# Performance work log

Measured on AMD Instinct MI355X. Metric: run time of the kernel, lower is better.

## Reference

```python
import jax, jax.numpy as jnp
import numpy as np
import math

B, C, MX, MY, MZ = 4, 64, 32, 32, 32
N_ATOM, EMB, N_HEAD = 64, 128, 8
HEAD = C // N_HEAD


def setup_inputs() -> dict:
    key = jax.random.key(0)
    ks = jax.random.split(key, 12)
    s = 0.05
    return {
        "x": jax.random.normal(ks[0], (B, C, MX, MY, MZ), jnp.float32),
        "mol_embed": jax.random.normal(ks[1], (B, N_ATOM, EMB), jnp.float32),
        "batch_nodes": jax.random.randint(ks[2], (B,), 1, N_ATOM + 1),  # >=1 valid atom
        "Wq": jax.random.normal(ks[3], (C, C), jnp.float32) * s,
        "bq": jnp.zeros((C,), jnp.float32),
        "Wk": jax.random.normal(ks[4], (C, EMB), jnp.float32) * s,
        "bk": jnp.zeros((C,), jnp.float32),
        "Wv": jax.random.normal(ks[5], (C, EMB), jnp.float32) * s,
        "bv": jnp.zeros((C,), jnp.float32),
        "Wo": jax.random.normal(ks[6], (C, C), jnp.float32) * s,
        "bo": jnp.zeros((C,), jnp.float32),
        "Wc": jax.random.normal(ks[7], (C, C, 3, 3, 3), jnp.float32) * s,
        "bc": jnp.zeros((C,), jnp.float32),
    }


def reference(x, mol_embed, batch_nodes, Wq, bq, Wk, bk, Wv, bv, Wo, bo, Wc, bc):
    b, c, mx, my, mz = x.shape
    m_voxel = mx * my * mz
    n_atom = mol_embed.shape[1]
    x_in = x

    # [b, m_voxel, c] voxel tokens
    xt = x.reshape(b, c, m_voxel).transpose(0, 2, 1)
    q = (xt @ Wq.T + bq).reshape(b, m_voxel, N_HEAD, HEAD)
    k = (mol_embed @ Wk.T + bk).reshape(b, n_atom, N_HEAD, HEAD)
    v = (mol_embed @ Wv.T + bv).reshape(b, n_atom, N_HEAD, HEAD)

    att = jnp.einsum('bqhd,bkhd->bhqk', q, k) / math.sqrt(HEAD)
    # ragged per-batch masking: atoms >= batch_nodes[i] are invalid
    valid = jnp.arange(n_atom)[None, :] < batch_nodes[:, None]  # [b, n_atom]
    att = jnp.where(valid[:, None, None, :], att, -jnp.inf)
    att = jax.nn.softmax(att, axis=-1)

    o = jnp.einsum('bhqk,bkhd->bqhd', att, v).reshape(b, m_voxel, c)
    o = jax.nn.relu(o @ Wo.T + bo)
    o = o.transpose(0, 2, 1).reshape(b, c, mx, my, mz)

    # conv3d k=3 with circular padding
    op = jnp.pad(o, ((0, 0), (0, 0), (1, 1), (1, 1), (1, 1)), mode='wrap')
    conv = jax.lax.conv_general_dilated(
        op, Wc, window_strides=(1, 1, 1), padding='VALID',
        dimension_numbers=('NCDHW', 'OIDHW', 'NCDHW'))
    conv = conv + bc[None, :, None, None, None]
    return jax.nn.relu(conv) + x_in
```

## Files before the change

### kernel.cpp

```cpp
#include <hip/hip_runtime.h>
#include <hip/hip_bf16.h>

#define B_    4
#define C_    64
#define MVOX  32768
#define NATOM 64
#define EMB_  128

typedef __attribute__((ext_vector_type(8)))  __bf16 bf16x8;
typedef __attribute__((ext_vector_type(4)))  float  f32x4;
typedef __attribute__((ext_vector_type(16))) float  f32x16;
typedef __attribute__((ext_vector_type(8)))  unsigned short ushort8;

typedef __attribute__((address_space(1))) const unsigned int gas_u32;
typedef __attribute__((address_space(3))) unsigned int las_u32;

static __device__ __forceinline__ unsigned short bf16u(float f) {
  __hip_bfloat16 h = __float2bfloat16(f);
  return *(unsigned short*)&h;
}

__global__ __launch_bounds__(256) void wprep_kernel(
    const float* __restrict__ Wc, const float* __restrict__ Wq,
    const float* __restrict__ Wo, const float* __restrict__ Wk,
    const float* __restrict__ Wv,
    __hip_bfloat16* __restrict__ Wt4, __hip_bfloat16* __restrict__ Wqb,
    __hip_bfloat16* __restrict__ Wob, __hip_bfloat16* __restrict__ Wkb,
    __hip_bfloat16* __restrict__ Wvb) {
  const int i = blockIdx.x * 256 + threadIdx.x;
  if (i < 110592) {
    const int tap = i >> 12;
    const int coh = (i >> 11) & 1;
    const int ks  = (i >> 9) & 3;
    const int l   = (i >> 3) & 63;
    const int j   = i & 7;
    const int co  = coh * 32 + (l & 31);
    const int ci  = ks * 16 + ((l >> 5) << 3) + j;
    Wt4[i] = __float2bfloat16(Wc[(co * C_ + ci) * 27 + tap]);
  } else if (i < 114688) {
    const int i2 = i - 110592;
    const int nf = (i2 >> 10) & 3;
    const int kk = (i2 >> 9) & 1;
    const int l  = (i2 >> 3) & 63;
    const int j  = i2 & 7;
    const int co = nf * 16 + (l & 15);
    const int ci = kk * 32 + ((l >> 4) << 3) + j;
    Wqb[i2] = __float2bfloat16(Wq[co * C_ + ci] * 0.3535533905932738f);
  } else if (i < 118784) {
    const int i3 = i - 114688;
    const int nf = (i3 >> 10) & 3;
    const int kk = (i3 >> 9) & 1;
    const int l  = (i3 >> 3) & 63;
    const int j  = i3 & 7;
    const int co = nf * 16 + (l & 15);
    const int ci = kk * 32 + ((l >> 4) << 3) + j;
    Wob[i3] = __float2bfloat16(Wo[co * C_ + ci]);
  } else if (i < 135168) {
    const int i4 = (i - 118784) & 8191;
    const bool is_v = (i - 118784) >= 8192;
    const int ch = i4 >> 12;
    const int kk = (i4 >> 9) & 7;
    const int l  = (i4 >> 3) & 63;
    const int j  = i4 & 7;
    const int c  = ch * 32 + (l & 31);
    const int e  = kk * 16 + ((l >> 5) << 3) + j;
    const float v = (is_v ? Wv : Wk)[c * EMB_ + e];
    (is_v ? Wvb : Wkb)[i4] = __float2bfloat16(v);
  }
}

__global__ __launch_bounds__(256) void kv_kernel(
    const float* __restrict__ mol,
    const __hip_bfloat16* __restrict__ Wkb, const float* __restrict__ bk,
    const __hip_bfloat16* __restrict__ Wvb, const float* __restrict__ bv,
    float* __restrict__ kout, float* __restrict__ vout) {
  __shared__ float smol[NATOM][132];

  const int b    = blockIdx.x;
  const int tid  = threadIdx.x;
  const int lane = tid & 63;
  const int w    = tid >> 6;
  const int kv   = w >> 1;
  const int ah   = w & 1;

  for (int i = tid; i < 2048; i += 256) {
    const int a = i >> 4, cb = (i & 15) * 8;
    const f32x4 v0 = *(const f32x4*)&mol[(size_t)(b * NATOM + a) * EMB_ + cb];
    const f32x4 v1 = *(const f32x4*)&mol[(size_t)(b * NATOM + a) * EMB_ + cb + 4];
    *(f32x4*)&smol[a][cb]     = v0;
    *(f32x4*)&smol[a][cb + 4] = v1;
  }
  __syncthreads();

  const __hip_bfloat16* Wb   = kv ? Wvb : Wkb;
  const float*          bias = kv ? bv : bk;
  float*                out  = kv ? vout : kout;

  f32x16 acc[2];
  #pragma unroll
  for (int ch = 0; ch < 2; ++ch)
    #pragma unroll
    for (int r = 0; r < 16; ++r) acc[ch][r] = 0.f;

  const int a  = ah * 32 + (lane & 31);
  #pragma unroll
  for (int kk = 0; kk < 8; ++kk) {
    const int e0 = kk * 16 + ((lane >> 5) << 3);
    ushort8 au;
    #pragma unroll
    for (int j = 0; j < 8; ++j) au[j] = bf16u(smol[a][e0 + j]);
    const bf16x8 af = __builtin_bit_cast(bf16x8, au);
    #pragma unroll
    for (int ch = 0; ch < 2; ++ch) {
      const bf16x8 bf = *(const bf16x8*)(Wb + (((ch * 8 + kk) << 6) + lane) * 8);
      acc[ch] = __builtin_amdgcn_mfma_f32_32x32x16_bf16(af, bf, acc[ch], 0, 0, 0);
    }
  }

  #pragma unroll
  for (int ch = 0; ch < 2; ++ch) {
    const int c = ch * 32 + (lane & 31);
    const float bb = bias[c];
    #pragma unroll
    for (int r = 0; r < 16; ++r) {
      const int ar = ah * 32 + (r & 3) + 8 * (r >> 2) + 4 * (lane >> 5);
      out[(size_t)(b * NATOM + ar) * C_ + c] = acc[ch][r] + bb;
    }
  }
}

__global__ __launch_bounds__(512, 4) void attn_kernel(
    const float* __restrict__ x,
    const float* __restrict__ kbuf, const float* __restrict__ vbuf,
    const int* __restrict__ batch_nodes,
    const __hip_bfloat16* __restrict__ Wqb, const float* __restrict__ bq,
    const __hip_bfloat16* __restrict__ Wob, const float* __restrict__ bo,
    __hip_bfloat16* __restrict__ omid) {
  __shared__ float sk[NATOM * C_];
  __shared__ float sv[NATOM * C_];
  __shared__ float xq[64 * C_];

  const int b    = blockIdx.y;
  const int m0   = blockIdx.x * 64;
  const int tid  = threadIdx.x;
  const int lane = tid & 63;
  const int w    = __builtin_amdgcn_readfirstlane(tid >> 6);
  const int h    = w;
  const int quad = lane >> 4;
  const int l15  = lane & 15;
  const int vq   = w & 3;
  const int cq   = w >> 2;

  #pragma unroll
  for (int j = 0; j < 2; ++j) {
    const int cidx = w * 2 + j;
    const int c  = cidx * 4 + (lane >> 4);
    const int v4 = (lane & 15) * 4;
    const float* gsrc = x + (size_t)(b * C_ + c) * MVOX + m0 + v4;
    __builtin_amdgcn_global_load_lds((gas_u32*)gsrc,
                                     (las_u32*)&xq[cidx * 256], 16, 0, 0);
  }
  for (int i = tid; i < NATOM * C_; i += 512) {
    const int at = i >> 6, c = i & 63;
    const int ad = (at << 6) + ((((c >> 2) ^ (at & 15)) << 2)) + (c & 3);
    sk[ad] = kbuf[b * NATOM * C_ + i];
    sv[ad] = vbuf[b * NATOM * C_ + i];
  }
  __syncthreads();

  f32x4 qacc[2];
  {
    bf16x8 af[2];
    #pragma unroll
    for (int kk = 0; kk < 2; ++kk) {
      ushort8 au;
      #pragma unroll
      for (int j = 0; j < 8; ++j)
        au[j] = bf16u(xq[(kk * 32 + quad * 8 + j) * 64 + vq * 16 + l15]);
      af[kk] = __builtin_bit_cast(bf16x8, au);
    }
    #pragma unroll
    for (int nf2 = 0; nf2 < 2; ++nf2) {
      const int nf = cq * 2 + nf2;
      const float bqv = bq[nf * 16 + l15] * 0.3535533905932738f;
      qacc[nf2] = {bqv, bqv, bqv, bqv};
      #pragma unroll
      for (int kk = 0; kk < 2; ++kk) {
        const bf16x8 bf = *(const bf16x8*)(Wqb + (((nf * 2 + kk) << 6) + lane) * 8);
        qacc[nf2] = __builtin_amdgcn_mfma_f32_16x16x32_bf16(af[kk], bf, qacc[nf2], 0, 0, 0);
      }
    }
  }
  __syncthreads();

  #pragma unroll
  for (int nf2 = 0; nf2 < 2; ++nf2) {
    const int co = (cq * 2 + nf2) * 16 + l15;
    const int c4 = co >> 2, ce = co & 3;
    #pragma unroll
    for (int r = 0; r < 4; ++r) {
      const int vr = vq * 16 + quad * 4 + r;
      xq[vr * 64 + ((c4 ^ (vr & 15)) << 2) + ce] = qacc[nf2][r];
    }
  }
  __syncthreads();

  const int nv = batch_nodes[b];

  bf16x8 kf[4];
  #pragma unroll
  for (int a = 0; a < 4; ++a) {
    const int arow = a * 16 + l15;
    const f32x4 k0 = *(const f32x4*)&sk[arow * 64 + (((2 * h)     ^ l15) << 2)];
    const f32x4 k1 = *(const f32x4*)&sk[arow * 64 + (((2 * h + 1) ^ l15) << 2)];
    ushort8 au;
    #pragma unroll
    for (int j = 0; j < 4; ++j) {
      au[j]     = (quad == 0) ? bf16u(k0[j]) : (unsigned short)0;
      au[4 + j] = (quad == 0) ? bf16u(k1[j]) : (unsigned short)0;
    }
    kf[a] = __builtin_bit_cast(bf16x8, au);
  }
  bf16x8 vf[2];
  {
    const int vc  = h * 8 + (l15 & 7);
    const int vc4 = vc >> 2, vce = vc & 3;
    #pragma unroll
    for (int s = 0; s < 2; ++s) {
      ushort8 au;
      #pragma unroll
      for (int j = 0; j < 8; ++j) {
        const int atom = (2 * s + (j >> 2)) * 16 + quad * 4 + (j & 3);
        au[j] = bf16u(sv[(atom << 6) + ((vc4 ^ (atom & 15)) << 2) + vce]);
      }
      vf[s] = __builtin_bit_cast(bf16x8, au);
    }
  }

  f32x4 oacc[4];
  #pragma unroll
  for (int v = 0; v < 4; ++v)
    #pragma unroll
    for (int r = 0; r < 4; ++r) oacc[v][r] = 0.f;

  const f32x4 zero4 = {0.f, 0.f, 0.f, 0.f};
  #pragma unroll
  for (int v = 0; v < 4; ++v) {
    const int qrow = v * 16 + l15;
    const f32x4 q0 = *(const f32x4*)&xq[qrow * 64 + (((2 * h)     ^ l15) << 2)];
    const f32x4 q1 = *(const f32x4*)&xq[qrow * 64 + (((2 * h + 1) ^ l15) << 2)];
    ushort8 qu;
    #pragma unroll
    for (int j = 0; j < 4; ++j) { qu[j] = bf16u(q0[j]); qu[4 + j] = bf16u(q1[j]); }
    const bf16x8 qf = __builtin_bit_cast(bf16x8, qu);

    f32x4 st[4];
    #pragma unroll
    for (int a = 0; a < 4; ++a)
      st[a] = __builtin_amdgcn_mfma_f32_16x16x32_bf16(kf[a], qf, zero4, 0, 0, 0);

    float m = -1e30f;
    #pragma unroll
    for (int a = 0; a < 4; ++a)
      #pragma unroll
      for (int r = 0; r < 4; ++r) {
        const int atom = a * 16 + quad * 4 + r;
        const float val = (atom < nv) ? st[a][r] : -1e30f;
        st[a][r] = val;
        m = fmaxf(m, val);
      }
    m = fmaxf(m, __shfl_xor(m, 16, 64));
    m = fmaxf(m, __shfl_xor(m, 32, 64));
    float ssum = 0.f;
    #pragma unroll
    for (int a = 0; a < 4; ++a)
      #pragma unroll
      for (int r = 0; r < 4; ++r) {
        const float p = __expf(st[a][r] - m);
        st[a][r] = p;
        ssum += p;
      }
    ssum += __shfl_xor(ssum, 16, 64);
    ssum += __shfl_xor(ssum, 32, 64);
    const float inv = 1.f / ssum;

    #pragma unroll
    for (int s = 0; s < 2; ++s) {
      ushort8 pu;
      #pragma unroll
      for (int j = 0; j < 8; ++j)
        pu[j] = bf16u(st[2 * s + (j >> 2)][j & 3] * inv);
      const bf16x8 pa = __builtin_bit_cast(bf16x8, pu);
      oacc[v] = __builtin_amdgcn_mfma_f32_16x16x32_bf16(pa, vf[s], oacc[v], 0, 0, 0);
    }
  }
  __syncthreads();

  float* os = sk;
  if (l15 < 8) {
    const int c = h * 8 + l15;
    const int c4 = c >> 2, ce = c & 3;
    #pragma unroll
    for (int v = 0; v < 4; ++v)
      #pragma unroll
      for (int r = 0; r < 4; ++r) {
        const int vxr = v * 16 + quad * 4 + r;
        os[vxr * 64 + ((c4 ^ (vxr & 15)) << 2) + ce] = oacc[v][r];
      }
  }
  __syncthreads();

  {
    bf16x8 af[2];
    #pragma unroll
    for (int kk = 0; kk < 2; ++kk) {
      ushort8 au;
      #pragma unroll
      for (int j = 0; j < 8; ++j) {
        const int ci = kk * 32 + quad * 8 + j;
        const int c4 = ci >> 2;
        au[j] = bf16u(os[(vq * 16 + l15) * 64 + ((c4 ^ l15) << 2) + (ci & 3)]);
      }
      af[kk] = __builtin_bit_cast(bf16x8, au);
    }
    f32x4 oac[2];
    #pragma unroll
    for (int nf2 = 0; nf2 < 2; ++nf2) {
      const int nf = cq * 2 + nf2;
      const float bov = bo[nf * 16 + l15];
      oac[nf2] = {bov, bov, bov, bov};
      #pragma unroll
      for (int kk = 0; kk < 2; ++kk) {
        const bf16x8 bf = *(const bf16x8*)(Wob + (((nf * 2 + kk) << 6) + lane) * 8);
        oac[nf2] = __builtin_amdgcn_mfma_f32_16x16x32_bf16(af[kk], bf, oac[nf2], 0, 0, 0);
      }
    }
    __syncthreads();
    unsigned short* osb = (unsigned short*)xq;
    #pragma unroll
    for (int nf2 = 0; nf2 < 2; ++nf2) {
      const int co = (cq * 2 + nf2) * 16 + l15;
      #pragma unroll
      for (int r = 0; r < 4; ++r) {
        const int vr = vq * 16 + quad * 4 + r;
        osb[vr * 64 + (((co >> 3) ^ (vr & 7)) << 3) + (co & 7)] =
            bf16u(fmaxf(oac[nf2][r], 0.f));
      }
    }
  }
  __syncthreads();

  *(ushort8*)(omid + (size_t)(b * MVOX + m0) * C_ + tid * 8) =
      *(const ushort8*)&((unsigned short*)xq)[tid * 8];
}

#define LOADB(dst, DX, DY, DZ)                                              \
  {                                                                         \
    const int zp_ = ((lane & 31) + (DZ) + 31) & 31;                         \
    const int sw_ = zp_ & 7;                                                \
    _Pragma("unroll")                                                       \
    for (int ks_ = 0; ks_ < 4; ++ks_) {                                     \
      const int phys_ = (ks_ * 2 + (lane >> 5)) ^ sw_;                      \
      _Pragma("unroll")                                                     \
      for (int i_ = 0; i_ < 2; ++i_) {                                      \
        const int hl_ = (lp + (DX)) * 4 + (i_ + (DY));                      \
        (dst)[i_ * 4 + ks_] =                                               \
            *(const bf16x8*)&halo[((hl_ * 32 + zp_) * 8 + phys_) * 8];      \
      }                                                                     \
    }                                                                       \
  }

#define LOADW(T2)                                                           \
  _Pragma("unroll")                                                         \
  for (int ks_ = 0; ks_ < 4; ++ks_)                                         \
    wf[(T2) % 3][ks_] =                                                     \
        *(const bf16x8*)(Wt4 + ((((T2) * 2 + coh) * 4 + ks_) << 9) + lane * 8);

#define DOMFMA(src, T)                                                      \
  _Pragma("unroll")                                                         \
  for (int ks_ = 0; ks_ < 4; ++ks_)                                         \
    _Pragma("unroll")                                                       \
    for (int i_ = 0; i_ < 2; ++i_)                                          \
      acc[i_] = __builtin_amdgcn_mfma_f32_32x32x16_bf16(                    \
          wf[(T) % 3][ks_], (src)[i_ * 4 + ks_], acc[i_], 0, 0, 0);

__global__ __launch_bounds__(256, 2) void conv_kernel(
    const __hip_bfloat16* __restrict__ omid,
    const __hip_bfloat16* __restrict__ Wt4,
    const float* __restrict__ bc,
    const float* __restrict__ xin,
    float* __restrict__ out) {
  __shared__ __hip_bfloat16 halo[512 * 64];

  const int b    = blockIdx.y;
  const int x0   = (blockIdx.x >> 4) * 2;
  const int y0   = (blockIdx.x & 15) * 2;
  const int tid  = threadIdx.x;
  const int lane = tid & 63;
  const int w    = tid >> 6;
  const int coh  = w & 1;
  const int lp   = w >> 1;

  {
    const __hip_bfloat16* src = omid + (size_t)b * MVOX * C_;
    #pragma unroll
    for (int n = 0; n < 16; ++n) {
      const int chunk = w * 16 + n;
      const int li = chunk >> 2;
      const int zb = (chunk & 3) * 8;
      const int gx = (x0 - 1 + (li >> 2)) & 31;
      const int gy = (y0 - 1 + (li & 3)) & 31;
      const __hip_bfloat16* gsrc = src + (size_t)(gx * 1024 + gy * 32 + zb) * C_ + lane * 8;
      __builtin_amdgcn_global_load_lds((gas_u32*)gsrc,
                                       (las_u32*)&halo[chunk * 512], 16, 0, 0);
    }
  }

  bf16x8 wf[3][4];
  LOADW(0);
  LOADW(1);
  __syncthreads();

  f32x16 acc[2];
  #pragma unroll
  for (int i = 0; i < 2; ++i)
    #pragma unroll
    for (int r = 0; r < 16; ++r) acc[i][r] = 0.f;

  bf16x8 bA[8], bB[8];
  LOADB(bA, 0, 0, 0);

  #pragma unroll
  for (int t = 0; t < 27; ++t) {
    const int dxn = (t + 1) / 9, dyn = ((t + 1) / 3) % 3, dzn = (t + 1) % 3;
    if ((t & 1) == 0) {
      if (t < 26) LOADB(bB, dxn, dyn, dzn);
      if (t < 25) LOADW(t + 2);
      DOMFMA(bA, t);
    } else {
      if (t < 26) LOADB(bA, dxn, dyn, dzn);
      if (t < 25) LOADW(t + 2);
      DOMFMA(bB, t);
    }
  }

  const int z = lane & 31;
  #pragma unroll
  for (int i = 0; i < 2; ++i) {
    const int gx = x0 + lp, gy = y0 + i;
    #pragma unroll
    for (int r = 0; r < 16; ++r) {
      const int co = coh * 32 + (r & 3) + 8 * (r >> 2) + 4 * (lane >> 5);
      const size_t idx = ((size_t)(b * C_ + co)) * MVOX + gx * 1024 + gy * 32 + z;
      out[idx] = fmaxf(acc[i][r] + bc[co], 0.f) + xin[idx];
    }
  }
}

extern "C" void kernel_launch(void* const* d_in, const int* in_sizes, int n_in,
                              void* d_out, int out_size, void* d_ws, size_t ws_size,
                              hipStream_t stream) {
  const float* x   = (const float*)d_in[0];
  const float* mol = (const float*)d_in[1];
  const int*   bn  = (const int*)  d_in[2];
  const float* Wq  = (const float*)d_in[3];
  const float* bq  = (const float*)d_in[4];
  const float* Wk  = (const float*)d_in[5];
  const float* bk  = (const float*)d_in[6];
  const float* Wv  = (const float*)d_in[7];
  const float* bv  = (const float*)d_in[8];
  const float* Wo  = (const float*)d_in[9];
  const float* bo  = (const float*)d_in[10];
  const float* Wc  = (const float*)d_in[11];
  const float* bc  = (const float*)d_in[12];
  float* out = (float*)d_out;

  char* ws = (char*)d_ws;
  __hip_bfloat16* omid = (__hip_bfloat16*)ws;
  float* kbuf = (float*)(ws + 16777216);
  float* vbuf = kbuf + B_ * NATOM * C_;
  __hip_bfloat16* Wt4 = (__hip_bfloat16*)(ws + 16908288);
  __hip_bfloat16* Wqb = (__hip_bfloat16*)(ws + 17129472);
  __hip_bfloat16* Wob = (__hip_bfloat16*)(ws + 17137664);
  __hip_bfloat16* Wkb = (__hip_bfloat16*)(ws + 17145856);
  __hip_bfloat16* Wvb = (__hip_bfloat16*)(ws + 17162240);

  wprep_kernel<<<dim3(528), 256, 0, stream>>>(Wc, Wq, Wo, Wk, Wv,
                                              Wt4, Wqb, Wob, Wkb, Wvb);
  kv_kernel<<<dim3(B_), 256, 0, stream>>>(mol, Wkb, bk, Wvb, bv, kbuf, vbuf);
  attn_kernel<<<dim3(MVOX / 64, B_), 512, 0, stream>>>(x, kbuf, vbuf, bn, Wqb, bq, Wob, bo, omid);
  conv_kernel<<<dim3(256, B_), 256, 0, stream>>>(omid, Wt4, bc, x, out);
}
```

Before: 88.69 us.

## Precompute K/V MFMA fragments in kv_kernel and shrink attention LDS usage

kv_kernel now writes K and V directly as bf16 MFMA-fragment-ordered buffers, so each attention block loads its per-head K/V fragments with a few vector global loads. This replaces the per-block staging of fp32 K/V into two 16KB shared arrays and the conversion work that went with it. Q and the attention output are stored in LDS as swizzled bf16 instead of fp32, so operands are read with single 16-byte loads and one barrier is dropped. Total LDS per block falls from 48KB to 16KB, which may raise occupancy. The cost is some extra rounding of intermediates to bf16 before the matmuls.

```diff
diff --git a/kernel.cpp b/kernel.cpp
--- a/kernel.cpp
+++ b/kernel.cpp
@@ -73,14 +73,15 @@
     const float* __restrict__ mol,
     const __hip_bfloat16* __restrict__ Wkb, const float* __restrict__ bk,
     const __hip_bfloat16* __restrict__ Wvb, const float* __restrict__ bv,
-    float* __restrict__ kout, float* __restrict__ vout) {
+    unsigned short* __restrict__ kfb, unsigned short* __restrict__ vfb) {
   __shared__ float smol[NATOM][132];
+  __shared__ float res[2][NATOM][68];
 
   const int b    = blockIdx.x;
   const int tid  = threadIdx.x;
   const int lane = tid & 63;
   const int w    = tid >> 6;
-  const int kv   = w >> 1;
+  const int kvw  = w >> 1;
   const int ah   = w & 1;
 
   for (int i = tid; i < 2048; i += 256) {
@@ -92,9 +93,8 @@
   }
   __syncthreads();
 
-  const __hip_bfloat16* Wb   = kv ? Wvb : Wkb;
-  const float*          bias = kv ? bv : bk;
-  float*                out  = kv ? vout : kout;
+  const __hip_bfloat16* Wb   = kvw ? Wvb : Wkb;
+  const float*          bias = kvw ? bv : bk;
 
   f32x16 acc[2];
   #pragma unroll
@@ -102,7 +102,7 @@
     #pragma unroll
     for (int r = 0; r < 16; ++r) acc[ch][r] = 0.f;
 
-  const int a  = ah * 32 + (lane & 31);
+  const int a = ah * 32 + (lane & 31);
   #pragma unroll
   for (int kk = 0; kk < 8; ++kk) {
     const int e0 = kk * 16 + ((lane >> 5) << 3);
@@ -124,21 +124,49 @@
     #pragma unroll
     for (int r = 0; r < 16; ++r) {
       const int ar = ah * 32 + (r & 3) + 8 * (r >> 2) + 4 * (lane >> 5);
-      out[(size_t)(b * NATOM + ar) * C_ + c] = acc[ch][r] + bb;
-    }
+      res[kvw][ar][c] = acc[ch][r] + bb;
+    }
+  }
+  __syncthreads();
+
+  #pragma unroll
+  for (int t = 0; t < 8; ++t) {
+    const int idx = t * 256 + tid;
+    const int h = idx >> 8, aa = (idx >> 6) & 3, ln = idx & 63;
+    const int qd = ln >> 4, l15 = ln & 15;
+    ushort8 au;
+    if (qd == 0) {
+      #pragma unroll
+      for (int j = 0; j < 8; ++j) au[j] = bf16u(res[0][aa * 16 + l15][h * 8 + j]);
+    } else {
+      #pragma unroll
+      for (int j = 0; j < 8; ++j) au[j] = 0;
+    }
+    *(ushort8*)(kfb + (size_t)(((b * 8 + h) * 4 + aa) * 64 + ln) * 8) = au;
+  }
+  #pragma unroll
+  for (int t = 0; t < 4; ++t) {
+    const int idx = t * 256 + tid;
+    const int h = idx >> 7, s = (idx >> 6) & 1, ln = idx & 63;
+    const int qd = ln >> 4, l15 = ln & 15;
+    ushort8 au;
+    #pragma unroll
+    for (int j = 0; j < 8; ++j) {
+      const int atom = (2 * s + (j >> 2)) * 16 + qd * 4 + (j & 3);
+      au[j] = bf16u(res[1][atom][h * 8 + (l15 & 7)]);
+    }
+    *(ushort8*)(vfb + (size_t)(((b * 8 + h) * 2 + s) * 64 + ln) * 8) = au;
   }
 }
 
 __global__ __launch_bounds__(512, 4) void attn_kernel(
     const float* __restrict__ x,
-    const float* __restrict__ kbuf, const float* __restrict__ vbuf,
+    const unsigned short* __restrict__ kfb, const unsigned short* __restrict__ vfb,
     const int* __restrict__ batch_nodes,
     const __hip_bfloat16* __restrict__ Wqb, const float* __restrict__ bq,
     const __hip_bfloat16* __restrict__ Wob, const float* __restrict__ bo,
     __hip_bfloat16* __restrict__ omid) {
-  __shared__ float sk[NATOM * C_];
-  __shared__ float sv[NATOM * C_];
-  __shared__ float xq[64 * C_];
+  __shared__ float buf[64 * C_];
 
   const int b    = blockIdx.y;
   const int m0   = blockIdx.x * 64;
@@ -151,6 +179,16 @@
   const int vq   = w & 3;
   const int cq   = w >> 2;
 
+  bf16x8 kf[4], vf[2];
+  #pragma unroll
+  for (int a = 0; a < 4; ++a)
+    kf[a] = __builtin_bit_cast(bf16x8,
+        *(const ushort8*)(kfb + (size_t)(((b * 8 + h) * 4 + a) * 64 + lane) * 8));
+  #pragma unroll
+  for (int s = 0; s < 2; ++s)
+    vf[s] = __builtin_bit_cast(bf16x8,
+        *(const ushort8*)(vfb + (size_t)(((b * 8 + h) * 2 + s) * 64 + lane) * 8));
+
   #pragma unroll
   for (int j = 0; j < 2; ++j) {
     const int cidx = w * 2 + j;
@@ -158,13 +196,7 @@
     const int v4 = (lane & 15) * 4;
     const float* gsrc = x + (size_t)(b * C_ + c) * MVOX + m0 + v4;
     __builtin_amdgcn_global_load_lds((gas_u32*)gsrc,
-                                     (las_u32*)&xq[cidx * 256], 16, 0, 0);
-  }
-  for (int i = tid; i < NATOM * C_; i += 512) {
-    const int at = i >> 6, c = i & 63;
-    const int ad = (at << 6) + ((((c >> 2) ^ (at & 15)) << 2)) + (c & 3);
-    sk[ad] = kbuf[b * NATOM * C_ + i];
-    sv[ad] = vbuf[b * NATOM * C_ + i];
+                                     (las_u32*)&buf[cidx * 256], 16, 0, 0);
   }
   __syncthreads();
 
@@ -176,7 +208,7 @@
       ushort8 au;
       #pragma unroll
       for (int j = 0; j < 8; ++j)
-        au[j] = bf16u(xq[(kk * 32 + quad * 8 + j) * 64 + vq * 16 + l15]);
+        au[j] = bf16u(buf[(kk * 32 + quad * 8 + j) * 64 + vq * 16 + l15]);
       af[kk] = __builtin_bit_cast(bf16x8, au);
     }
     #pragma unroll
@@ -193,49 +225,20 @@
   }
   __syncthreads();
 
+  unsigned short* qb = (unsigned short*)buf;
   #pragma unroll
   for (int nf2 = 0; nf2 < 2; ++nf2) {
     const int co = (cq * 2 + nf2) * 16 + l15;
-    const int c4 = co >> 2, ce = co & 3;
     #pragma unroll
     for (int r = 0; r < 4; ++r) {
       const int vr = vq * 16 + quad * 4 + r;
-      xq[vr * 64 + ((c4 ^ (vr & 15)) << 2) + ce] = qacc[nf2][r];
+      qb[vr * 64 + (((co >> 3) ^ (vr & 7)) << 3) + (co & 7)] = bf16u(qacc[nf2][r]);
     }
   }
   __syncthreads();
 
   const int nv = batch_nodes[b];
-
-  bf16x8 kf[4];
-  #pragma unroll
-  for (int a = 0; a < 4; ++a) {
-    const int arow = a * 16 + l15;
-    const f32x4 k0 = *(const f32x4*)&sk[arow * 64 + (((2 * h)     ^ l15) << 2)];
-    const f32x4 k1 = *(const f32x4*)&sk[arow * 64 + (((2 * h + 1) ^ l15) << 2)];
-    ushort8 au;
-    #pragma unroll
-    for (int j = 0; j < 4; ++j) {
-      au[j]     = (quad == 0) ? bf16u(k0[j]) : (unsigned short)0;
-      au[4 + j] = (quad == 0) ? bf16u(k1[j]) : (unsigned short)0;
-    }
-    kf[a] = __builtin_bit_cast(bf16x8, au);
-  }
-  bf16x8 vf[2];
-  {
-    const int vc  = h * 8 + (l15 & 7);
-    const int vc4 = vc >> 2, vce = vc & 3;
-    #pragma unroll
-    for (int s = 0; s < 2; ++s) {
-      ushort8 au;
-      #pragma unroll
-      for (int j = 0; j < 8; ++j) {
-        const int atom = (2 * s + (j >> 2)) * 16 + quad * 4 + (j & 3);
-        au[j] = bf16u(sv[(atom << 6) + ((vc4 ^ (atom & 15)) << 2) + vce]);
-      }
-      vf[s] = __builtin_bit_cast(bf16x8, au);
-    }
-  }
+  unsigned short* ob = (unsigned short*)buf + 4096;
 
   f32x4 oacc[4];
   #pragma unroll
@@ -247,12 +250,8 @@
   #pragma unroll
   for (int v = 0; v < 4; ++v) {
     const int qrow = v * 16 + l15;
-    const f32x4 q0 = *(const f32x4*)&xq[qrow * 64 + (((2 * h)     ^ l15) << 2)];
-    const f32x4 q1 = *(const f32x4*)&xq[qrow * 64 + (((2 * h + 1) ^ l15) << 2)];
-    ushort8 qu;
-    #pragma unroll
-    for (int j = 0; j < 4; ++j) { qu[j] = bf16u(q0[j]); qu[4 + j] = bf16u(q1[j]); }
-    const bf16x8 qf = __builtin_bit_cast(bf16x8, qu);
+    const bf16x8 qf = __builtin_bit_cast(bf16x8,
+        *(const ushort8*)&qb[qrow * 64 + ((h ^ (qrow & 7)) << 3)]);
 
     f32x4 st[4];
     #pragma unroll
@@ -294,18 +293,15 @@
       oacc[v] = __builtin_amdgcn_mfma_f32_16x16x32_bf16(pa, vf[s], oacc[v], 0, 0, 0);
     }
   }
-  __syncthreads();
-
-  float* os = sk;
+
   if (l15 < 8) {
     const int c = h * 8 + l15;
-    const int c4 = c >> 2, ce = c & 3;
     #pragma unroll
     for (int v = 0; v < 4; ++v)
       #pragma unroll
       for (int r = 0; r < 4; ++r) {
         const int vxr = v * 16 + quad * 4 + r;
-        os[vxr * 64 + ((c4 ^ (vxr & 15)) << 2) + ce] = oacc[v][r];
+        ob[vxr * 64 + ((h ^ (vxr & 7)) << 3) + l15] = bf16u(oacc[v][r]);
       }
   }
   __syncthreads();
@@ -314,14 +310,9 @@
     bf16x8 af[2];
     #pragma unroll
     for (int kk = 0; kk < 2; ++kk) {
-      ushort8 au;
-      #pragma unroll
-      for (int j = 0; j < 8; ++j) {
-        const int ci = kk * 32 + quad * 8 + j;
-        const int c4 = ci >> 2;
-        au[j] = bf16u(os[(vq * 16 + l15) * 64 + ((c4 ^ l15) << 2) + (ci & 3)]);
-      }
-      af[kk] = __builtin_bit_cast(bf16x8, au);
+      const int row = vq * 16 + l15;
+      af[kk] = __builtin_bit_cast(bf16x8,
+          *(const ushort8*)&ob[row * 64 + (((kk * 4 + quad) ^ (row & 7)) << 3)]);
     }
     f32x4 oac[2];
     #pragma unroll
@@ -336,7 +327,7 @@
       }
     }
     __syncthreads();
-    unsigned short* osb = (unsigned short*)xq;
+    unsigned short* osb = (unsigned short*)buf;
     #pragma unroll
     for (int nf2 = 0; nf2 < 2; ++nf2) {
       const int co = (cq * 2 + nf2) * 16 + l15;
@@ -351,7 +342,7 @@
   __syncthreads();
 
   *(ushort8*)(omid + (size_t)(b * MVOX + m0) * C_ + tid * 8) =
-      *(const ushort8*)&((unsigned short*)xq)[tid * 8];
+      *(const ushort8*)&((unsigned short*)buf)[tid * 8];
 }
 
 #define LOADB(dst, DX, DY, DZ)                                              \
@@ -477,17 +468,17 @@
 
   char* ws = (char*)d_ws;
   __hip_bfloat16* omid = (__hip_bfloat16*)ws;
-  float* kbuf = (float*)(ws + 16777216);
-  float* vbuf = kbuf + B_ * NATOM * C_;
-  __hip_bfloat16* Wt4 = (__hip_bfloat16*)(ws + 16908288);
-  __hip_bfloat16* Wqb = (__hip_bfloat16*)(ws + 17129472);
-  __hip_bfloat16* Wob = (__hip_bfloat16*)(ws + 17137664);
-  __hip_bfloat16* Wkb = (__hip_bfloat16*)(ws + 17145856);
-  __hip_bfloat16* Wvb = (__hip_bfloat16*)(ws + 17162240);
+  __hip_bfloat16* Wt4  = (__hip_bfloat16*)(ws + 16777216);
+  __hip_bfloat16* Wqb  = (__hip_bfloat16*)(ws + 16998400);
+  __hip_bfloat16* Wob  = (__hip_bfloat16*)(ws + 17006592);
+  __hip_bfloat16* Wkb  = (__hip_bfloat16*)(ws + 17014784);
+  __hip_bfloat16* Wvb  = (__hip_bfloat16*)(ws + 17031168);
+  unsigned short* kfb  = (unsigned short*)(ws + 17047552);
+  unsigned short* vfb  = (unsigned short*)(ws + 17178624);
 
   wprep_kernel<<<dim3(528), 256, 0, stream>>>(Wc, Wq, Wo, Wk, Wv,
                                               Wt4, Wqb, Wob, Wkb, Wvb);
-  kv_kernel<<<dim3(B_), 256, 0, stream>>>(mol, Wkb, bk, Wvb, bv, kbuf, vbuf);
-  attn_kernel<<<dim3(MVOX / 64, B_), 512, 0, stream>>>(x, kbuf, vbuf, bn, Wqb, bq, Wob, bo, omid);
+  kv_kernel<<<dim3(B_), 256, 0, stream>>>(mol, Wkb, bk, Wvb, bv, kfb, vfb);
+  attn_kernel<<<dim3(MVOX / 64, B_), 512, 0, stream>>>(x, kfb, vfb, bn, Wqb, bq, Wob, bo, omid);
   conv_kernel<<<dim3(256, B_), 256, 0, stream>>>(omid, Wt4, bc, x, out);
 }
```

New measurement: 83.39 us. -6.0%, faster.
